# Kernel tuning notes

Hardware: AMD Instinct MI355X
Metric: run time of the kernel (lower is better)

Reference implementation:

```python
import jax, jax.numpy as jnp
import numpy as np

B, S, HOPS, DIM, NREL = 1024, 32, 2, 64, 237
NENT, NEDGE = 14541, 272115
SIGMA = 0.1
CFMW = 64


def setup_inputs() -> dict:
    key = jax.random.key(0)
    ks = jax.random.split(key, 20)

    def g(k, shape):
        return (jax.random.normal(k, shape, dtype=jnp.float32) / np.float32(np.sqrt(shape[0])))

    inp = {
        "entity_pairs": jax.random.randint(ks[0], (B, 2), 0, NENT),
        "train_edges": jax.random.randint(ks[1], (B,), 0, NEDGE),
        "labels": jax.random.randint(ks[2], (B,), 0, NREL),
        "entity2edges": jax.random.randint(ks[3], (NENT + 1, S), 0, NEDGE + 1),
        "edge2entities": jax.random.randint(ks[4], (NEDGE + 1, 1), 0, NENT + 1),
        "edge2relation": jax.random.randint(ks[5], (NEDGE + 1,), 0, NREL + 1),
        "t": jax.random.uniform(ks[6], (B,), dtype=jnp.float32),
        "eps": jax.random.normal(ks[7], (B, NREL), dtype=jnp.float32),
        "rel_feat": g(ks[8], (NREL, DIM)),
        "W_agg0": g(ks[9], (DIM, DIM)), "b_agg0": jnp.zeros((DIM,), jnp.float32),
        "W_agg1": g(ks[10], (DIM, NREL)), "b_agg1": jnp.zeros((NREL,), jnp.float32),
        "W_out": g(ks[11], (2 * NREL, NREL)), "b_out": jnp.zeros((NREL,), jnp.float32),
        "mW1": g(ks[12], (NREL + 1, CFMW)), "mb1": jnp.zeros((CFMW,), jnp.float32),
        "mW2": g(ks[13], (CFMW, CFMW)), "mb2": jnp.zeros((CFMW,), jnp.float32),
        "mW3": g(ks[14], (CFMW, CFMW)), "mb3": jnp.zeros((CFMW,), jnp.float32),
        "mW4": g(ks[15], (CFMW, NREL)), "mb4": jnp.zeros((NREL,), jnp.float32),
    }
    return inp


def _side(ent, labels, train_edges, entity2edges, edge2entities, edge2relation, relf, aggs):
    # multi-hop neighbor edge gather + masks (exclude the training edge itself)
    edges_list = [labels]  # hop-0 "edges" are the relation labels
    masks = []
    for i in range(HOPS):
        if i == 0:
            ne = ent.reshape(B, 1)  # (B, 1) source entities
        else:
            ne = edge2entities[edges_list[-1].reshape(-1)].reshape(B, -1)
        nedges = entity2edges[ne.reshape(-1)].reshape(B, -1)  # (B, S**(i+1))
        edges_list.append(nedges)
        masks.append((nedges != train_edges[:, None]).astype(relf.dtype))
    # edge -> relation -> feature
    ev = [relf[edges_list[0]]]  # (B, DIM)
    for edges in edges_list[1:]:
        ev.append(relf[edge2relation[edges]])  # (B, S**h, DIM)
    # iterative mean aggregation (PathCon-style, one entity per edge)
    for i in range(HOPS):
        W, b, act, self_inc = aggs[i]
        d = W.shape[0]
        nxt = []
        for hop in range(HOPS - i):
            neigh = ev[hop + 1].reshape(B, -1, 1, S, d)
            m = masks[hop].reshape(B, -1, 1, S, 1)
            out = jnp.mean(jnp.mean(neigh * m, axis=-2), axis=-2)  # (B, S**hop, d)
            if self_inc:
                out = out + ev[hop].reshape(B, -1, d)
            nxt.append(act(out @ W + b))
        ev = nxt
    return ev[0].reshape(B, NREL)


def reference(entity_pairs, train_edges, labels, entity2edges, edge2entities,
              edge2relation, t, eps, rel_feat, W_agg0, b_agg0, W_agg1, b_agg1,
              W_out, b_out, mW1, mb1, mW2, mb2, mW3, mb3, mW4, mb4):
    relf = jnp.concatenate([rel_feat, jnp.zeros((1, DIM), rel_feat.dtype)], axis=0)
    aggs = [
        (W_agg0, b_agg0, jax.nn.relu, True),    # intermediate hop: relu, self-included
        (W_agg1, b_agg1, lambda x: x, False),   # last hop: identity, no self
    ]
    x0 = _side(entity_pairs[:, 0], labels, train_edges, entity2edges,
               edge2entities, edge2relation, relf, aggs)
    x1 = _side(entity_pairs[:, 1], labels, train_edges, entity2edges,
               edge2entities, edge2relation, relf, aggs)
    output = jnp.concatenate([x0, x1], axis=-1) @ W_out + b_out  # (B, NREL)
    # CFM: xt = (1-t) x0 + t x1 + sigma*eps ; ut = x1 - x0
    tb = t[:, None]
    xt = (1.0 - tb) * x0 + tb * x1 + SIGMA * eps
    h = jnp.concatenate([xt, tb], axis=-1)
    h = jax.nn.selu(h @ mW1 + mb1)
    h = jax.nn.selu(h @ mW2 + mb2)
    h = jax.nn.selu(h @ mW3 + mb3)
    vt = h @ mW4 + mb4
    scores = output * vt
    return scores
```

## Files before the change

### kernel.cpp

```cpp
#include <hip/hip_runtime.h>
#include <math.h>

#define BB 1024
#define S 32
#define DIM 64
#define NREL 237
#define NENT 14541
#define SIGMA 0.1f

#define OFS_WR    0
#define N_WR      (238*64)
#define OFS_WC0   15232
#define N_WC      (64*237)
#define OFS_WC1   (OFS_WC0 + N_WC)
#define OFS_BC    (OFS_WC1 + N_WC)
#define OFS_A     45872
#define OFS_WM    976560
#define OFS_PE    980656

#define LDS_BYTES 18688

__device__ __forceinline__ float selu_f(float x) {
    const float alpha = 1.6732632423543772f;
    const float scale = 1.0507009873554805f;
    return scale * (x > 0.f ? x : alpha * expm1f(x));
}

__global__ __launch_bounds__(512) void pre_kernel(
    const float* __restrict__ rel_feat, const float* __restrict__ W0,
    const float* __restrict__ W1, const float* __restrict__ mW1,
    const float* __restrict__ b1, const float* __restrict__ mb1,
    const float* __restrict__ eps,
    float* __restrict__ ws) {
    __shared__ float sm[2160];
    int blk = blockIdx.x;
    const int tid = threadIdx.x;

    if (blk < 30) {
        int idx = blk * 512 + tid;
        if (idx < 238 * 64) {
            int r = idx >> 6, o = idx & 63;
            float acc = 0.f;
            if (r < NREL) {
#pragma unroll 8
                for (int d = 0; d < 64; ++d)
                    acc += rel_feat[r * 64 + d] * W0[d * 64 + o];
            }
            ws[OFS_WR + idx] = acc;
        }
        return;
    }
    blk -= 30;
    if (blk < 8) {
        int o0 = blk * 8;
        const float* src = W1 + o0 * 237;
        for (int i = tid; i < 8 * 237; i += 512) sm[i] = src[i];
        __syncthreads();
        int w = tid >> 6, cl = tid & 63;
        const float* row = sm + w * 237;
        float a0 = 0.f, a1 = 0.f, a2 = 0.f, a3 = 0.f;
#pragma unroll
        for (int k = 0; k < 236; k += 4) {
            a0 += row[k]     * mW1[k * 64 + cl];
            a1 += row[k + 1] * mW1[(k + 1) * 64 + cl];
            a2 += row[k + 2] * mW1[(k + 2) * 64 + cl];
            a3 += row[k + 3] * mW1[(k + 3) * 64 + cl];
        }
        a0 += row[236] * mW1[236 * 64 + cl];
        ws[OFS_WM + (o0 + w) * 64 + cl] = (a0 + a1) + (a2 + a3);
        return;
    }
    blk -= 8;
    {
        int b0 = blk * 8;
        const float* esrc = eps + b0 * 237;
        for (int i = tid; i < 8 * 237; i += 512) sm[i] = esrc[i];
        for (int i = tid; i < 237; i += 512) sm[1920 + i] = b1[i];
        __syncthreads();
        int w = tid >> 6, cl = tid & 63;
        const float* ew = sm + w * 237;
        const float* bb = sm + 1920;
        float a0 = mb1[cl], a1 = 0.f, a2 = 0.f, a3 = 0.f;
#pragma unroll
        for (int k = 0; k < 236; k += 4) {
            a0 += (SIGMA * ew[k]     + bb[k])     * mW1[k * 64 + cl];
            a1 += (SIGMA * ew[k + 1] + bb[k + 1]) * mW1[(k + 1) * 64 + cl];
            a2 += (SIGMA * ew[k + 2] + bb[k + 2]) * mW1[(k + 2) * 64 + cl];
            a3 += (SIGMA * ew[k + 3] + bb[k + 3]) * mW1[(k + 3) * 64 + cl];
        }
        a0 += (SIGMA * ew[236] + bb[236]) * mW1[236 * 64 + cl];
        ws[OFS_PE + (b0 + w) * 64 + cl] = (a0 + a1) + (a2 + a3);
    }
}

__global__ __launch_bounds__(512) void mid_kernel(
    const int* __restrict__ e2e_tab, const int* __restrict__ e2r,
    const float* __restrict__ W1, const float* __restrict__ b1,
    const float* __restrict__ W_out, const float* __restrict__ b_out,
    float* __restrict__ ws) {
    __shared__ int   s_r[1024];
    __shared__ float red[512];
    int blk = blockIdx.x;
    const int tid = threadIdx.x;

    if (blk < 455) {
        const int grp = tid >> 4, c = tid & 15;
        const int ent = blk * 32 + grp;
        const bool ok = ent < (NENT + 1);
        if (ok) {
            int ea = e2e_tab[ent * S + c];
            int eb = e2e_tab[ent * S + 16 + c];
            s_r[grp * 32 + c] = e2r[ea];
            s_r[grp * 32 + 16 + c] = e2r[eb];
        }
        __syncthreads();
        if (ok) {
            const float4* Wr4 = (const float4*)(ws + OFS_WR);
            const int* rr = &s_r[grp * 32];
            float4 acc = make_float4(0.f, 0.f, 0.f, 0.f);
#pragma unroll
            for (int s = 0; s < 32; ++s) {
                float4 v = Wr4[rr[s] * 16 + c];
                acc.x += v.x; acc.y += v.y; acc.z += v.z; acc.w += v.w;
            }
            ((float4*)(ws + OFS_A))[ent * 16 + c] = acc;
        }
        return;
    }
    blk -= 455;
    if (blk < 512) {
        int half = blk >> 8;
        int lb = blk & 255;
        int o = lb >> 2, ct = lb & 3;
        int cl = tid & 63, q = tid >> 6;
        int c = ct * 64 + cl;
        const float* Wsrc = W_out + half * 237 * 237;
        float acc = 0.f;
        if (c < NREL) {
            int k0 = q * 30, k1 = (q == 7) ? 237 : (k0 + 30);
#pragma unroll 4
            for (int k = k0; k < k1; ++k)
                acc += W1[o * 237 + k] * Wsrc[k * 237 + c];
        }
        red[tid] = acc;
        __syncthreads();
        if (q == 0 && c < NREL) {
            float s = 0.f;
#pragma unroll
            for (int qq = 0; qq < 8; ++qq) s += red[qq * 64 + cl];
            ws[(half ? OFS_WC1 : OFS_WC0) + o * 237 + c] = s;
        }
        return;
    }
    blk -= 512;
    {
        int cl = tid & 63, q = tid >> 6;
        int c = blk * 64 + cl;
        float acc = 0.f;
        if (c < NREL) {
            int k0 = q * 30, k1 = (q == 7) ? 237 : (k0 + 30);
#pragma unroll 4
            for (int k = k0; k < k1; ++k)
                acc += b1[k] * (W_out[k * 237 + c] + W_out[(237 + k) * 237 + c]);
        }
        red[tid] = acc;
        __syncthreads();
        if (q == 0 && c < NREL) {
            float s = b_out[c];
#pragma unroll
            for (int qq = 0; qq < 8; ++qq) s += red[qq * 64 + cl];
            ws[OFS_BC + c] = s;
        }
    }
}

__global__ __launch_bounds__(512, 8) void gf_kernel(
    const int* __restrict__ ep, const int* __restrict__ te_arr,
    const int* __restrict__ e2e_tab, const int* __restrict__ e2ent,
    const int* __restrict__ e2r, const float* __restrict__ b0,
    const float* __restrict__ t_arr,
    const float* __restrict__ mW1,
    const float* __restrict__ mW2, const float* __restrict__ mb2,
    const float* __restrict__ mW3, const float* __restrict__ mb3,
    const float* __restrict__ mW4, const float* __restrict__ mb4,
    const float* __restrict__ ws, float* __restrict__ out) {
    extern __shared__ float smem[];
    float* s_v1   = smem;
    int*   s_r1   = (int*)(smem + 4352);
    int*   s_ent2 = (int*)(smem + 4416);
    float* s_m1   = smem + 4480;
    float* s_ov   = smem + 4544;

    const int tid = threadIdx.x;
    const int b = blockIdx.x;
    const int grp = tid >> 4;
    const int c = tid & 15;
    const int te = te_arr[b];
    const int rte = e2r[te];
    const float4* Wr4 = (const float4*)(ws + OFS_WR);
    const float4* A4  = (const float4*)(ws + OFS_A);
    const float4 b0v  = ((const float4*)b0)[c];
    const float4 wrte = Wr4[rte * 16 + c];

    if (tid < 64) {
        int u = tid >> 5, s = tid & 31;
        int ent = ep[b * 2 + u];
        int e1 = e2e_tab[ent * S + s];
        s_r1[u * 32 + s] = e2r[e1];
        s_m1[u * 32 + s] = (e1 != te) ? 1.0f : 0.0f;
        s_ent2[u * 32 + s] = e2ent[e1];
    }
    __syncthreads();

    const float inv = 1.0f / 32.0f;
#pragma unroll
    for (int u = 0; u < 2; ++u) {
        const int j = grp;
        const int ent2 = s_ent2[u * 32 + j];
        int e2a = e2e_tab[ent2 * S + c];
        int e2b = e2e_tab[ent2 * S + 16 + c];
        int cnt = (e2a == te) + (e2b == te);
        cnt += __shfl_xor(cnt, 1);
        cnt += __shfl_xor(cnt, 2);
        cnt += __shfl_xor(cnt, 4);
        cnt += __shfl_xor(cnt, 8);
        float4 a4   = A4[ent2 * 16 + c];
        float4 self = Wr4[s_r1[u * 32 + j] * 16 + c];
        float fc = (float)cnt;
        float m = s_m1[u * 32 + j];
        float4 r;
        r.x = fmaxf(self.x + (a4.x - fc * wrte.x) * inv + b0v.x, 0.f) * m;
        r.y = fmaxf(self.y + (a4.y - fc * wrte.y) * inv + b0v.y, 0.f) * m;
        r.z = fmaxf(self.z + (a4.z - fc * wrte.z) * inv + b0v.z, 0.f) * m;
        r.w = fmaxf(self.w + (a4.w - fc * wrte.w) * inv + b0v.w, 0.f) * m;
        *((float4*)&s_v1[(u * 32 + j) * 68 + c * 4]) = r;
    }
    __syncthreads();
    if (tid < 128) {
        int u = tid >> 6, w = tid & 63;
        float sum = 0.f;
#pragma unroll 8
        for (int j = 0; j < 32; ++j) sum += s_v1[(u * 32 + j) * 68 + w];
        s_ov[u * 64 + w] = sum * inv;
    }
    __syncthreads();

    float* s_outp = smem;
    float* s_vp   = smem + 480;
    float* s_hA   = smem + 960;
    float* s_hB   = smem + 1024;
    float* s_omix = smem + 1088;
    const float tb = t_arr[b];
    const float* Wc0 = ws + OFS_WC0;
    const float* Wc1 = ws + OFS_WC1;
    const float* bc  = ws + OFS_BC;
    const float* Wm  = ws + OFS_WM;
    const float* pe  = ws + OFS_PE + b * 64;

    if (tid < 64)
        s_omix[tid] = (1.f - tb) * s_ov[tid] + tb * s_ov[64 + tid];
    {
        int half = tid >> 8, cc = tid & 255;
        if (cc < NREL) {
            const float* Wc  = half ? Wc1 : Wc0;
            const float* ovp = s_ov + half * 64;
            float a = 0.f;
#pragma unroll 4
            for (int d = 0; d < 64; ++d)
                a += ovp[d] * Wc[d * 237 + cc];
            s_outp[half * 240 + cc] = a;
        }
    }
    __syncthreads();

    if (tid < 64) {
        float a0 = pe[tid] + tb * mW1[237 * 64 + tid];
        float a1 = 0.f, a2 = 0.f, a3 = 0.f;
#pragma unroll
        for (int d = 0; d < 64; d += 4) {
            a0 += s_omix[d]     * Wm[d * 64 + tid];
            a1 += s_omix[d + 1] * Wm[(d + 1) * 64 + tid];
            a2 += s_omix[d + 2] * Wm[(d + 2) * 64 + tid];
            a3 += s_omix[d + 3] * Wm[(d + 3) * 64 + tid];
        }
        s_hA[tid] = selu_f((a0 + a1) + (a2 + a3));
    }
    __syncthreads();

    if (tid < 64) {
        float a0 = mb2[tid], a1 = 0.f, a2 = 0.f, a3 = 0.f;
#pragma unroll
        for (int d = 0; d < 64; d += 4) {
            a0 += s_hA[d]     * mW2[d * 64 + tid];
            a1 += s_hA[d + 1] * mW2[(d + 1) * 64 + tid];
            a2 += s_hA[d + 2] * mW2[(d + 2) * 64 + tid];
            a3 += s_hA[d + 3] * mW2[(d + 3) * 64 + tid];
        }
        s_hB[tid] = selu_f((a0 + a1) + (a2 + a3));
    }
    __syncthreads();

    if (tid < 64) {
        float a0 = mb3[tid], a1 = 0.f, a2 = 0.f, a3 = 0.f;
#pragma unroll
        for (int d = 0; d < 64; d += 4) {
            a0 += s_hB[d]     * mW3[d * 64 + tid];
            a1 += s_hB[d + 1] * mW3[(d + 1) * 64 + tid];
            a2 += s_hB[d + 2] * mW3[(d + 2) * 64 + tid];
            a3 += s_hB[d + 3] * mW3[(d + 3) * 64 + tid];
        }
        s_hA[tid] = selu_f((a0 + a1) + (a2 + a3));
    }
    __syncthreads();

    {
        int half = tid >> 8, cc = tid & 255;
        if (cc < NREL) {
            float a = 0.f;
#pragma unroll 4
            for (int w = half * 32; w < half * 32 + 32; ++w)
                a += s_hA[w] * mW4[w * 237 + cc];
            s_vp[half * 240 + cc] = a;
        }
    }
    __syncthreads();

    if (tid < NREL) {
        float outv = bc[tid] + s_outp[tid] + s_outp[240 + tid];
        out[b * 237 + tid] = outv * (mb4[tid] + s_vp[tid] + s_vp[240 + tid]);
    }
}

extern "C" void kernel_launch(void* const* d_in, const int* in_sizes, int n_in,
                              void* d_out, int out_size, void* d_ws, size_t ws_size,
                              hipStream_t stream) {
    const int* ep       = (const int*)d_in[0];
    const int* te       = (const int*)d_in[1];
    const int* e2e      = (const int*)d_in[3];
    const int* e2ent    = (const int*)d_in[4];
    const int* e2r      = (const int*)d_in[5];
    const float* t      = (const float*)d_in[6];
    const float* eps    = (const float*)d_in[7];
    const float* relf   = (const float*)d_in[8];
    const float* W0     = (const float*)d_in[9];
    const float* b0     = (const float*)d_in[10];
    const float* W1     = (const float*)d_in[11];
    const float* b1     = (const float*)d_in[12];
    const float* W_out  = (const float*)d_in[13];
    const float* b_out  = (const float*)d_in[14];
    const float* mW1    = (const float*)d_in[15];
    const float* mb1    = (const float*)d_in[16];
    const float* mW2    = (const float*)d_in[17];
    const float* mb2    = (const float*)d_in[18];
    const float* mW3    = (const float*)d_in[19];
    const float* mb3    = (const float*)d_in[20];
    const float* mW4    = (const float*)d_in[21];
    const float* mb4    = (const float*)d_in[22];
    float* ws  = (float*)d_ws;
    float* out = (float*)d_out;

    hipLaunchKernelGGL(pre_kernel, dim3(166), dim3(512), 0, stream,
                       relf, W0, W1, mW1, b1, mb1, eps, ws);
    hipLaunchKernelGGL(mid_kernel, dim3(971), dim3(512), 0, stream,
                       e2e, e2r, W1, b1, W_out, b_out, ws);
    hipLaunchKernelGGL(gf_kernel, dim3(BB), dim3(512), LDS_BYTES, stream,
                       ep, te, e2e, e2ent, e2r, b0,
                       t, mW1, mW2, mb2, mW3, mb3, mW4, mb4, ws, out);
}
```

Measured before the change: 137.6 us.

## Drop per-entity neighbor-sum precompute; aggregate only needed entities inside main kernel

Removes the precompute pass that summed projected relation features over all ~14.5k entities and instead computes the 32-edge aggregate on the fly for only the 64 second-hop entities each batch row needs. The remaining precompute work is merged into a single prep kernel, removing one launch and one inter-kernel dependency. The main kernel now stages second-hop edge ids and relations in LDS (more LDS per block, which may lower occupancy) and performs 32 gathered float4 loads per thread instead of one.

New measurement: 151.4 us. 1.1x slower.

```diff
diff --git a/kernel.cpp b/kernel.cpp
--- a/kernel.cpp
+++ b/kernel.cpp
@@ -14,11 +14,10 @@
 #define N_WC      (64*237)
 #define OFS_WC1   (OFS_WC0 + N_WC)
 #define OFS_BC    (OFS_WC1 + N_WC)
-#define OFS_A     45872
 #define OFS_WM    976560
 #define OFS_PE    980656
 
-#define LDS_BYTES 18688
+#define LDS_BYTES 35584
 
 __device__ __forceinline__ float selu_f(float x) {
     const float alpha = 1.6732632423543772f;
@@ -26,109 +25,19 @@
     return scale * (x > 0.f ? x : alpha * expm1f(x));
 }
 
-__global__ __launch_bounds__(512) void pre_kernel(
+__global__ __launch_bounds__(512) void prep_kernel(
     const float* __restrict__ rel_feat, const float* __restrict__ W0,
-    const float* __restrict__ W1, const float* __restrict__ mW1,
-    const float* __restrict__ b1, const float* __restrict__ mb1,
+    const float* __restrict__ W1, const float* __restrict__ b1,
+    const float* __restrict__ W_out, const float* __restrict__ b_out,
+    const float* __restrict__ mW1, const float* __restrict__ mb1,
     const float* __restrict__ eps,
     float* __restrict__ ws) {
     __shared__ float sm[2160];
     int blk = blockIdx.x;
     const int tid = threadIdx.x;
 
-    if (blk < 30) {
-        int idx = blk * 512 + tid;
-        if (idx < 238 * 64) {
-            int r = idx >> 6, o = idx & 63;
-            float acc = 0.f;
-            if (r < NREL) {
-#pragma unroll 8
-                for (int d = 0; d < 64; ++d)
-                    acc += rel_feat[r * 64 + d] * W0[d * 64 + o];
-            }
-            ws[OFS_WR + idx] = acc;
-        }
-        return;
-    }
-    blk -= 30;
-    if (blk < 8) {
-        int o0 = blk * 8;
-        const float* src = W1 + o0 * 237;
-        for (int i = tid; i < 8 * 237; i += 512) sm[i] = src[i];
-        __syncthreads();
-        int w = tid >> 6, cl = tid & 63;
-        const float* row = sm + w * 237;
-        float a0 = 0.f, a1 = 0.f, a2 = 0.f, a3 = 0.f;
-#pragma unroll
-        for (int k = 0; k < 236; k += 4) {
-            a0 += row[k]     * mW1[k * 64 + cl];
-            a1 += row[k + 1] * mW1[(k + 1) * 64 + cl];
-            a2 += row[k + 2] * mW1[(k + 2) * 64 + cl];
-            a3 += row[k + 3] * mW1[(k + 3) * 64 + cl];
-        }
-        a0 += row[236] * mW1[236 * 64 + cl];
-        ws[OFS_WM + (o0 + w) * 64 + cl] = (a0 + a1) + (a2 + a3);
-        return;
-    }
-    blk -= 8;
-    {
-        int b0 = blk * 8;
-        const float* esrc = eps + b0 * 237;
-        for (int i = tid; i < 8 * 237; i += 512) sm[i] = esrc[i];
-        for (int i = tid; i < 237; i += 512) sm[1920 + i] = b1[i];
-        __syncthreads();
-        int w = tid >> 6, cl = tid & 63;
-        const float* ew = sm + w * 237;
-        const float* bb = sm + 1920;
-        float a0 = mb1[cl], a1 = 0.f, a2 = 0.f, a3 = 0.f;
-#pragma unroll
-        for (int k = 0; k < 236; k += 4) {
-            a0 += (SIGMA * ew[k]     + bb[k])     * mW1[k * 64 + cl];
-            a1 += (SIGMA * ew[k + 1] + bb[k + 1]) * mW1[(k + 1) * 64 + cl];
-            a2 += (SIGMA * ew[k + 2] + bb[k + 2]) * mW1[(k + 2) * 64 + cl];
-            a3 += (SIGMA * ew[k + 3] + bb[k + 3]) * mW1[(k + 3) * 64 + cl];
-        }
-        a0 += (SIGMA * ew[236] + bb[236]) * mW1[236 * 64 + cl];
-        ws[OFS_PE + (b0 + w) * 64 + cl] = (a0 + a1) + (a2 + a3);
-    }
-}
-
-__global__ __launch_bounds__(512) void mid_kernel(
-    const int* __restrict__ e2e_tab, const int* __restrict__ e2r,
-    const float* __restrict__ W1, const float* __restrict__ b1,
-    const float* __restrict__ W_out, const float* __restrict__ b_out,
-    float* __restrict__ ws) {
-    __shared__ int   s_r[1024];
-    __shared__ float red[512];
-    int blk = blockIdx.x;
-    const int tid = threadIdx.x;
-
-    if (blk < 455) {
-        const int grp = tid >> 4, c = tid & 15;
-        const int ent = blk * 32 + grp;
-        const bool ok = ent < (NENT + 1);
-        if (ok) {
-            int ea = e2e_tab[ent * S + c];
-            int eb = e2e_tab[ent * S + 16 + c];
-            s_r[grp * 32 + c] = e2r[ea];
-            s_r[grp * 32 + 16 + c] = e2r[eb];
-        }
-        __syncthreads();
-        if (ok) {
-            const float4* Wr4 = (const float4*)(ws + OFS_WR);
-            const int* rr = &s_r[grp * 32];
-            float4 acc = make_float4(0.f, 0.f, 0.f, 0.f);
-#pragma unroll
-            for (int s = 0; s < 32; ++s) {
-                float4 v = Wr4[rr[s] * 16 + c];
-                acc.x += v.x; acc.y += v.y; acc.z += v.z; acc.w += v.w;
-            }
-            ((float4*)(ws + OFS_A))[ent * 16 + c] = acc;
-        }
-        return;
-    }
-    blk -= 455;
     if (blk < 512) {
+        float* red = sm;
         int half = blk >> 8;
         int lb = blk & 255;
         int o = lb >> 2, ct = lb & 3;
@@ -153,7 +62,8 @@
         return;
     }
     blk -= 512;
-    {
+    if (blk < 4) {
+        float* red = sm;
         int cl = tid & 63, q = tid >> 6;
         int c = blk * 64 + cl;
         float acc = 0.f;
@@ -171,6 +81,63 @@
             for (int qq = 0; qq < 8; ++qq) s += red[qq * 64 + cl];
             ws[OFS_BC + c] = s;
         }
+        return;
+    }
+    blk -= 4;
+    if (blk < 30) {
+        int idx = blk * 512 + tid;
+        if (idx < 238 * 64) {
+            int r = idx >> 6, o = idx & 63;
+            float acc = 0.f;
+            if (r < NREL) {
+#pragma unroll 8
+                for (int d = 0; d < 64; ++d)
+                    acc += rel_feat[r * 64 + d] * W0[d * 64 + o];
+            }
+            ws[OFS_WR + idx] = acc;
+        }
+        return;
+    }
+    blk -= 30;
+    if (blk < 8) {
+        int o0 = blk * 8;
+        const float* src = W1 + o0 * 237;
+        for (int i = tid; i < 8 * 237; i += 512) sm[i] = src[i];
+        __syncthreads();
+        int w = tid >> 6, cl = tid & 63;
+        const float* row = sm + w * 237;
+        float a0 = 0.f, a1 = 0.f, a2 = 0.f, a3 = 0.f;
+#pragma unroll
+        for (int k = 0; k < 236; k += 4) {
+            a0 += row[k]     * mW1[k * 64 + cl];
+            a1 += row[k + 1] * mW1[(k + 1) * 64 + cl];
+            a2 += row[k + 2] * mW1[(k + 2) * 64 + cl];
+            a3 += row[k + 3] * mW1[(k + 3) * 64 + cl];
+        }
+        a0 += row[236] * mW1[236 * 64 + cl];
+        ws[OFS_WM + (o0 + w) * 64 + cl] = (a0 + a1) + (a2 + a3);
+        return;
+    }
+    blk -= 8;
+    {
+        int b0 = blk * 8;
+        const float* esrc = eps + b0 * 237;
+        for (int i = tid; i < 8 * 237; i += 512) sm[i] = esrc[i];
+        for (int i = tid; i < 237; i += 512) sm[1920 + i] = b1[i];
+        __syncthreads();
+        int w = tid >> 6, cl = tid & 63;
+        const float* ew = sm + w * 237;
+        const float* bb = sm + 1920;
+        float a0 = mb1[cl], a1 = 0.f, a2 = 0.f, a3 = 0.f;
+#pragma unroll
+        for (int k = 0; k < 236; k += 4) {
+            a0 += (SIGMA * ew[k]     + bb[k])     * mW1[k * 64 + cl];
+            a1 += (SIGMA * ew[k + 1] + bb[k + 1]) * mW1[(k + 1) * 64 + cl];
+            a2 += (SIGMA * ew[k + 2] + bb[k + 2]) * mW1[(k + 2) * 64 + cl];
+            a3 += (SIGMA * ew[k + 3] + bb[k + 3]) * mW1[(k + 3) * 64 + cl];
+        }
+        a0 += (SIGMA * ew[236] + bb[236]) * mW1[236 * 64 + cl];
+        ws[OFS_PE + (b0 + w) * 64 + cl] = (a0 + a1) + (a2 + a3);
     }
 }
 
@@ -190,6 +157,8 @@
     int*   s_ent2 = (int*)(smem + 4416);
     float* s_m1   = smem + 4480;
     float* s_ov   = smem + 4544;
+    int*   s_e    = (int*)(smem + 4672);
+    int*   s_r2   = (int*)(smem + 6784);
 
     const int tid = threadIdx.x;
     const int b = blockIdx.x;
@@ -198,7 +167,6 @@
     const int te = te_arr[b];
     const int rte = e2r[te];
     const float4* Wr4 = (const float4*)(ws + OFS_WR);
-    const float4* A4  = (const float4*)(ws + OFS_A);
     const float4 b0v  = ((const float4*)b0)[c];
     const float4 wrte = Wr4[rte * 16 + c];
 
@@ -212,28 +180,47 @@
     }
     __syncthreads();
 
+#pragma unroll
+    for (int k = 0; k < 4; ++k) {
+        int idx = k * 512 + tid;
+        int g = idx >> 5;
+        int s = idx & 31;
+        int ent2 = s_ent2[g];
+        int e = e2e_tab[ent2 * S + s];
+        s_e[g * 33 + s] = e;
+        s_r2[g * 33 + s] = e2r[e];
+    }
+    __syncthreads();
+
     const float inv = 1.0f / 32.0f;
 #pragma unroll
     for (int u = 0; u < 2; ++u) {
         const int j = grp;
-        const int ent2 = s_ent2[u * 32 + j];
-        int e2a = e2e_tab[ent2 * S + c];
-        int e2b = e2e_tab[ent2 * S + 16 + c];
+        const int g = u * 32 + j;
+        const int* eg = s_e + g * 33;
+        const int* rg = s_r2 + g * 33;
+        int e2a = eg[c];
+        int e2b = eg[16 + c];
         int cnt = (e2a == te) + (e2b == te);
         cnt += __shfl_xor(cnt, 1);
         cnt += __shfl_xor(cnt, 2);
         cnt += __shfl_xor(cnt, 4);
         cnt += __shfl_xor(cnt, 8);
-        float4 a4   = A4[ent2 * 16 + c];
-        float4 self = Wr4[s_r1[u * 32 + j] * 16 + c];
+        float4 a4 = make_float4(0.f, 0.f, 0.f, 0.f);
+#pragma unroll
+        for (int s = 0; s < 32; ++s) {
+            float4 v = Wr4[rg[s] * 16 + c];
+            a4.x += v.x; a4.y += v.y; a4.z += v.z; a4.w += v.w;
+        }
+        float4 self = Wr4[s_r1[g] * 16 + c];
         float fc = (float)cnt;
-        float m = s_m1[u * 32 + j];
+        float m = s_m1[g];
         float4 r;
         r.x = fmaxf(self.x + (a4.x - fc * wrte.x) * inv + b0v.x, 0.f) * m;
         r.y = fmaxf(self.y + (a4.y - fc * wrte.y) * inv + b0v.y, 0.f) * m;
         r.z = fmaxf(self.z + (a4.z - fc * wrte.z) * inv + b0v.z, 0.f) * m;
         r.w = fmaxf(self.w + (a4.w - fc * wrte.w) * inv + b0v.w, 0.f) * m;
-        *((float4*)&s_v1[(u * 32 + j) * 68 + c * 4]) = r;
+        *((float4*)&s_v1[g * 68 + c * 4]) = r;
     }
     __syncthreads();
     if (tid < 128) {
@@ -359,10 +346,8 @@
     float* ws  = (float*)d_ws;
     float* out = (float*)d_out;
 
-    hipLaunchKernelGGL(pre_kernel, dim3(166), dim3(512), 0, stream,
-                       relf, W0, W1, mW1, b1, mb1, eps, ws);
-    hipLaunchKernelGGL(mid_kernel, dim3(971), dim3(512), 0, stream,
-                       e2e, e2r, W1, b1, W_out, b_out, ws);
+    hipLaunchKernelGGL(prep_kernel, dim3(682), dim3(512), 0, stream,
+                       relf, W0, W1, b1, W_out, b_out, mW1, mb1, eps, ws);
     hipLaunchKernelGGL(gf_kernel, dim3(BB), dim3(512), LDS_BYTES, stream,
                        ep, te, e2e, e2ent, e2r, b0,
                        t, mW1, mW2, mb2, mW3, mb3, mW4, mb4, ws, out);
```

## Pack edge tables and per-entity aggregates into combined records for gather locality

Applied to the files above, without the earlier changes.

Packs edge2entity and edge2relation into a single int per edge (entity in low bits, relation in high bits) in a new pre_kernel section. mid_kernel now writes per-entity records that hold the aggregated feature sum next to that entity's 32 edge ids. The final kernel then reads one contiguous record per neighbour entity instead of separate e2e, A and e2r/e2ent gathers. This cuts the number of scattered memory transactions in the gather-heavy kernel. The cost is an extra packing pass over roughly 272K edges and a larger workspace footprint.

Result: slower. 140.6 us (+2.2%).

```diff
diff --git a/kernel.cpp b/kernel.cpp
--- a/kernel.cpp
+++ b/kernel.cpp
@@ -9,14 +9,13 @@
 #define SIGMA 0.1f
 
 #define OFS_WR    0
-#define N_WR      (238*64)
 #define OFS_WC0   15232
-#define N_WC      (64*237)
-#define OFS_WC1   (OFS_WC0 + N_WC)
-#define OFS_BC    (OFS_WC1 + N_WC)
-#define OFS_A     45872
-#define OFS_WM    976560
-#define OFS_PE    980656
+#define OFS_WC1   30400
+#define OFS_BC    45568
+#define OFS_WM    45808
+#define OFS_PE    49904
+#define OFS_EE    115440
+#define OFS_REC   387584
 
 #define LDS_BYTES 18688
 
@@ -31,11 +30,54 @@
     const float* __restrict__ W1, const float* __restrict__ mW1,
     const float* __restrict__ b1, const float* __restrict__ mb1,
     const float* __restrict__ eps,
+    const int* __restrict__ e2r, const int* __restrict__ e2ent,
     float* __restrict__ ws) {
     __shared__ float sm[2160];
     int blk = blockIdx.x;
     const int tid = threadIdx.x;
 
+    if (blk < 128) {
+        int b0 = blk * 8;
+        const float* esrc = eps + b0 * 237;
+        for (int i = tid; i < 8 * 237; i += 512) sm[i] = esrc[i];
+        for (int i = tid; i < 237; i += 512) sm[1920 + i] = b1[i];
+        __syncthreads();
+        int w = tid >> 6, cl = tid & 63;
+        const float* ew = sm + w * 237;
+        const float* bb = sm + 1920;
+        float a0 = mb1[cl], a1 = 0.f, a2 = 0.f, a3 = 0.f;
+#pragma unroll
+        for (int k = 0; k < 236; k += 4) {
+            a0 += (SIGMA * ew[k]     + bb[k])     * mW1[k * 64 + cl];
+            a1 += (SIGMA * ew[k + 1] + bb[k + 1]) * mW1[(k + 1) * 64 + cl];
+            a2 += (SIGMA * ew[k + 2] + bb[k + 2]) * mW1[(k + 2) * 64 + cl];
+            a3 += (SIGMA * ew[k + 3] + bb[k + 3]) * mW1[(k + 3) * 64 + cl];
+        }
+        a0 += (SIGMA * ew[236] + bb[236]) * mW1[236 * 64 + cl];
+        ws[OFS_PE + (b0 + w) * 64 + cl] = (a0 + a1) + (a2 + a3);
+        return;
+    }
+    blk -= 128;
+    if (blk < 8) {
+        int o0 = blk * 8;
+        const float* src = W1 + o0 * 237;
+        for (int i = tid; i < 8 * 237; i += 512) sm[i] = src[i];
+        __syncthreads();
+        int w = tid >> 6, cl = tid & 63;
+        const float* row = sm + w * 237;
+        float a0 = 0.f, a1 = 0.f, a2 = 0.f, a3 = 0.f;
+#pragma unroll
+        for (int k = 0; k < 236; k += 4) {
+            a0 += row[k]     * mW1[k * 64 + cl];
+            a1 += row[k + 1] * mW1[(k + 1) * 64 + cl];
+            a2 += row[k + 2] * mW1[(k + 2) * 64 + cl];
+            a3 += row[k + 3] * mW1[(k + 3) * 64 + cl];
+        }
+        a0 += row[236] * mW1[236 * 64 + cl];
+        ws[OFS_WM + (o0 + w) * 64 + cl] = (a0 + a1) + (a2 + a3);
+        return;
+    }
+    blk -= 8;
     if (blk < 30) {
         int idx = blk * 512 + tid;
         if (idx < 238 * 64) {
@@ -51,45 +93,18 @@
         return;
     }
     blk -= 30;
-    if (blk < 8) {
-        int o0 = blk * 8;
-        const float* src = W1 + o0 * 237;
-        for (int i = tid; i < 8 * 237; i += 512) sm[i] = src[i];
-        __syncthreads();
-        int w = tid >> 6, cl = tid & 63;
-        const float* row = sm + w * 237;
-        float a0 = 0.f, a1 = 0.f, a2 = 0.f, a3 = 0.f;
-#pragma unroll
-        for (int k = 0; k < 236; k += 4) {
-            a0 += row[k]     * mW1[k * 64 + cl];
-            a1 += row[k + 1] * mW1[(k + 1) * 64 + cl];
-            a2 += row[k + 2] * mW1[(k + 2) * 64 + cl];
-            a3 += row[k + 3] * mW1[(k + 3) * 64 + cl];
-        }
-        a0 += row[236] * mW1[236 * 64 + cl];
-        ws[OFS_WM + (o0 + w) * 64 + cl] = (a0 + a1) + (a2 + a3);
-        return;
-    }
-    blk -= 8;
     {
-        int b0 = blk * 8;
-        const float* esrc = eps + b0 * 237;
-        for (int i = tid; i < 8 * 237; i += 512) sm[i] = esrc[i];
-        for (int i = tid; i < 237; i += 512) sm[1920 + i] = b1[i];
-        __syncthreads();
-        int w = tid >> 6, cl = tid & 63;
-        const float* ew = sm + w * 237;
-        const float* bb = sm + 1920;
-        float a0 = mb1[cl], a1 = 0.f, a2 = 0.f, a3 = 0.f;
-#pragma unroll
-        for (int k = 0; k < 236; k += 4) {
-            a0 += (SIGMA * ew[k]     + bb[k])     * mW1[k * 64 + cl];
-            a1 += (SIGMA * ew[k + 1] + bb[k + 1]) * mW1[(k + 1) * 64 + cl];
-            a2 += (SIGMA * ew[k + 2] + bb[k + 2]) * mW1[(k + 2) * 64 + cl];
-            a3 += (SIGMA * ew[k + 3] + bb[k + 3]) * mW1[(k + 3) * 64 + cl];
-        }
-        a0 += (SIGMA * ew[236] + bb[236]) * mW1[236 * 64 + cl];
-        ws[OFS_PE + (b0 + w) * 64 + cl] = (a0 + a1) + (a2 + a3);
+        int i = blk * 512 + tid;
+        if (i < 68029) {
+            int4 r = ((const int4*)e2r)[i];
+            int4 e = ((const int4*)e2ent)[i];
+            int4 p;
+            p.x = (e.x & 0x3FFF) | (r.x << 16);
+            p.y = (e.y & 0x3FFF) | (r.y << 16);
+            p.z = (e.z & 0x3FFF) | (r.z << 16);
+            p.w = (e.w & 0x3FFF) | (r.w << 16);
+            ((int4*)((int*)ws + OFS_EE))[i] = p;
+        }
     }
 }
 
@@ -107,9 +122,10 @@
         const int grp = tid >> 4, c = tid & 15;
         const int ent = blk * 32 + grp;
         const bool ok = ent < (NENT + 1);
+        int ea = 0, eb = 0;
         if (ok) {
-            int ea = e2e_tab[ent * S + c];
-            int eb = e2e_tab[ent * S + 16 + c];
+            ea = e2e_tab[ent * S + c];
+            eb = e2e_tab[ent * S + 16 + c];
             s_r[grp * 32 + c] = e2r[ea];
             s_r[grp * 32 + 16 + c] = e2r[eb];
         }
@@ -123,7 +139,11 @@
                 float4 v = Wr4[rr[s] * 16 + c];
                 acc.x += v.x; acc.y += v.y; acc.z += v.z; acc.w += v.w;
             }
-            ((float4*)(ws + OFS_A))[ent * 16 + c] = acc;
+            float* rec = ws + OFS_REC + ent * 96;
+            ((float4*)rec)[c] = acc;
+            int* recE = (int*)rec + 64;
+            recE[2 * c]     = ea;
+            recE[2 * c + 1] = eb;
         }
         return;
     }
@@ -176,9 +196,7 @@
 
 __global__ __launch_bounds__(512, 8) void gf_kernel(
     const int* __restrict__ ep, const int* __restrict__ te_arr,
-    const int* __restrict__ e2e_tab, const int* __restrict__ e2ent,
-    const int* __restrict__ e2r, const float* __restrict__ b0,
-    const float* __restrict__ t_arr,
+    const float* __restrict__ b0, const float* __restrict__ t_arr,
     const float* __restrict__ mW1,
     const float* __restrict__ mW2, const float* __restrict__ mb2,
     const float* __restrict__ mW3, const float* __restrict__ mb3,
@@ -196,19 +214,22 @@
     const int grp = tid >> 4;
     const int c = tid & 15;
     const int te = te_arr[b];
-    const int rte = e2r[te];
+    const int* ee = (const int*)ws + OFS_EE;
+    const float* REC = ws + OFS_REC;
+    const int rte = ee[te] >> 16;
     const float4* Wr4 = (const float4*)(ws + OFS_WR);
-    const float4* A4  = (const float4*)(ws + OFS_A);
     const float4 b0v  = ((const float4*)b0)[c];
     const float4 wrte = Wr4[rte * 16 + c];
 
     if (tid < 64) {
         int u = tid >> 5, s = tid & 31;
         int ent = ep[b * 2 + u];
-        int e1 = e2e_tab[ent * S + s];
-        s_r1[u * 32 + s] = e2r[e1];
+        const int* er = (const int*)(REC + ent * 96) + 64;
+        int e1 = er[(s < 16) ? (2 * s) : (2 * (s - 16) + 1)];
+        int p = ee[e1];
+        s_r1[u * 32 + s] = p >> 16;
         s_m1[u * 32 + s] = (e1 != te) ? 1.0f : 0.0f;
-        s_ent2[u * 32 + s] = e2ent[e1];
+        s_ent2[u * 32 + s] = p & 0x3FFF;
     }
     __syncthreads();
 
@@ -217,14 +238,14 @@
     for (int u = 0; u < 2; ++u) {
         const int j = grp;
         const int ent2 = s_ent2[u * 32 + j];
-        int e2a = e2e_tab[ent2 * S + c];
-        int e2b = e2e_tab[ent2 * S + 16 + c];
-        int cnt = (e2a == te) + (e2b == te);
+        const float* rec = REC + ent2 * 96;
+        float4 a4 = ((const float4*)rec)[c];
+        int2 e2 = *((const int2*)((const int*)rec + 64) + c);
+        int cnt = (e2.x == te) + (e2.y == te);
         cnt += __shfl_xor(cnt, 1);
         cnt += __shfl_xor(cnt, 2);
         cnt += __shfl_xor(cnt, 4);
         cnt += __shfl_xor(cnt, 8);
-        float4 a4   = A4[ent2 * 16 + c];
         float4 self = Wr4[s_r1[u * 32 + j] * 16 + c];
         float fc = (float)cnt;
         float m = s_m1[u * 32 + j];
@@ -359,11 +380,11 @@
     float* ws  = (float*)d_ws;
     float* out = (float*)d_out;
 
-    hipLaunchKernelGGL(pre_kernel, dim3(166), dim3(512), 0, stream,
-                       relf, W0, W1, mW1, b1, mb1, eps, ws);
+    hipLaunchKernelGGL(pre_kernel, dim3(299), dim3(512), 0, stream,
+                       relf, W0, W1, mW1, b1, mb1, eps, e2r, e2ent, ws);
     hipLaunchKernelGGL(mid_kernel, dim3(971), dim3(512), 0, stream,
                        e2e, e2r, W1, b1, W_out, b_out, ws);
     hipLaunchKernelGGL(gf_kernel, dim3(BB), dim3(512), LDS_BYTES, stream,
-                       ep, te, e2e, e2ent, e2r, b0,
-                       t, mW1, mW2, mb2, mW3, mb3, mW4, mb4, ws, out);
-}
+                       ep, te, b0, t, mW1, mW2, mb2, mW3, mb3, mW4, mb4,
+                       ws, out);
+}
```
